# Kernel tuning notes

Hardware: AMD Instinct MI355X
Metric: run time of the kernel (lower is better)

## Reference

```python
import jax, jax.numpy as jnp
import numpy as np

N = 8192
D = 128
NUM_CLASSES = 100
EPS = 1e-8  # torch CosineSimilarity default eps


def _l2_normalize(x):
    # torch cosine sim divides by max(||x||, eps)
    n = jnp.sqrt(jnp.sum(x * x, axis=-1, keepdims=True))
    return x / jnp.maximum(n, EPS)


def _remove_diag(M):
    # [n, n] -> [n, n-1], dropping the diagonal, no boolean gather needed
    n = M.shape[0]
    return M.reshape(-1)[1:].reshape(n - 1, n + 1)[:, :-1].reshape(n, n - 1)


def setup_inputs() -> dict:
    key = jax.random.key(0)
    k1, k2, k3, k4 = jax.random.split(key, 4)
    inst_embed = jax.random.normal(k1, (N, D), dtype=jnp.float32)
    proxy = jax.random.normal(k2, (N, D), dtype=jnp.float32)
    negative_mask = jax.random.randint(k3, (NUM_CLASSES, N), 0, 2).astype(jnp.float32)
    labels = jax.random.randint(k4, (N,), 0, NUM_CLASSES, dtype=jnp.int64) if jax.config.jax_enable_x64 else jax.random.randint(k4, (N,), 0, NUM_CLASSES, dtype=jnp.int32)
    return {
        "inst_embed": inst_embed,
        "proxy": proxy,
        "negative_mask": negative_mask,
        "labels": labels,
        "temperature": jnp.float32(0.07),
        "margin": jnp.float32(0.0),
    }


def reference(inst_embed, proxy, negative_mask, labels, temperature, margin):
    xn = _l2_normalize(inst_embed)                       # [N, D]
    # pairwise cosine similarity via normalize + matmul (not NxNxD broadcast)
    sim = xn @ xn.T                                      # [N, N]
    instance_zone = jnp.exp((_remove_diag(sim) - margin) / temperature)  # [N, N-1]

    pn = _l2_normalize(proxy)
    inst2proxy_positive = jnp.exp((jnp.sum(xn * pn, axis=-1) - margin) / temperature)  # [N]

    # pos_collected_numerator == True branch
    mask = _remove_diag(negative_mask[labels])           # [N, N-1]
    numerator = jnp.sum(instance_zone * mask, axis=1) + inst2proxy_positive
    denominator = inst2proxy_positive + jnp.sum(instance_zone, axis=1)
    return -jnp.mean(jnp.log(numerator / denominator))
```

## Files before the change

kernel.cpp:

```cpp
#include <hip/hip_runtime.h>
#include <stdint.h>

#define NROWS 8192
#define DD 128
#define EPS 1e-8f
#define LOG2E 1.4426950408889634f

#define SPLIT 16
#define RPB 128
#define CPT 32
#define LDS_COL 272
#define NT ((NROWS / SPLIT) / CPT)
#define NORM_BLOCKS (NROWS / 4)
#define PACK_BLOCKS 3200

typedef __bf16 bf16x8 __attribute__((ext_vector_type(8)));
typedef float f32x4 __attribute__((ext_vector_type(4)));

__device__ __forceinline__ unsigned int f2bf(float f) {
  union { float f; unsigned int u; } v; v.f = f;
  unsigned int u = v.u;
  return (u + 0x7fffu + ((u >> 16) & 1u)) >> 16;
}
__device__ __forceinline__ float bf2f(unsigned int b) {
  union { unsigned int u; float f; } v; v.u = b << 16;
  return v.f;
}

__global__ __launch_bounds__(256) void norm_kernel(
    const float* __restrict__ x, const float* __restrict__ pr,
    const float* __restrict__ nm, const int* __restrict__ lb,
    const float* __restrict__ tptr,
    unsigned short* __restrict__ xnA, unsigned short* __restrict__ xnB,
    float* __restrict__ p, float* __restrict__ eself, float* __restrict__ mii,
    float* __restrict__ tot, float* __restrict__ msk,
    unsigned int* __restrict__ packed, float* __restrict__ out)
{
  int wave = threadIdx.x >> 6, lane = threadIdx.x & 63;
  int bx = blockIdx.x;

  if (bx >= NORM_BLOCKS) {
    int widx = (bx - NORM_BLOCKS) * 4 + wave;
    int cls = widx >> 7;
    int w64 = widx & 127;
    float v = nm[(size_t)cls * NROWS + w64 * 64 + lane];
    unsigned long long b = __ballot(v != 0.0f);
    if (lane == 0) {
      packed[cls * 256 + w64 * 2] = (unsigned int)b;
      packed[cls * 256 + w64 * 2 + 1] = (unsigned int)(b >> 32);
    }
    return;
  }

  int row = bx * 4 + wave;
  float2 xv = ((const float2*)(x + (size_t)row * DD))[lane];
  float2 pv = ((const float2*)(pr + (size_t)row * DD))[lane];
  float sx = xv.x * xv.x + xv.y * xv.y;
  float sp = pv.x * pv.x + pv.y * pv.y;
  float dp = xv.x * pv.x + xv.y * pv.y;
  #pragma unroll
  for (int m = 1; m < 64; m <<= 1) {
    sx += __shfl_xor(sx, m);
    sp += __shfl_xor(sp, m);
    dp += __shfl_xor(dp, m);
  }
  float inx = 1.f / fmaxf(sqrtf(sx), EPS);
  float inp = 1.f / fmaxf(sqrtf(sp), EPS);
  float s1 = LOG2E / tptr[0];

  unsigned int a0 = f2bf(xv.x * inx * s1), a1 = f2bf(xv.y * inx * s1);
  unsigned int b0 = f2bf(xv.x * inx),      b1 = f2bf(xv.y * inx);
  ((unsigned int*)(xnA + (size_t)row * DD))[lane] = a0 | (a1 << 16);
  ((unsigned int*)(xnB + (size_t)row * DD))[lane] = b0 | (b1 << 16);

  float ss = bf2f(a0) * bf2f(b0) + bf2f(a1) * bf2f(b1);
  #pragma unroll
  for (int m = 1; m < 64; m <<= 1) ss += __shfl_xor(ss, m);

  if (lane == 0) {
    p[row] = __builtin_amdgcn_exp2f(dp * inx * inp * s1);
    eself[row] = __builtin_amdgcn_exp2f(ss);
    mii[row] = nm[(size_t)lb[row] * NROWS + row];
    tot[row] = 0.f;
    msk[row] = 0.f;
    if (row == 0) out[0] = 0.f;
  }
}

__global__ __launch_bounds__(256, 4) void main_kernel(
    const unsigned short* __restrict__ xnA_u, const unsigned short* __restrict__ xnB_u,
    const unsigned int* __restrict__ packed, const int* __restrict__ labels,
    float* __restrict__ tot, float* __restrict__ msk)
{
  __shared__ unsigned char lds[2][CPT * LDS_COL];
  int tid = threadIdx.x;
  int wave = tid >> 6, lane = tid & 63;
  int q = lane >> 4, c = lane & 15;
  int rb0 = blockIdx.x * RPB + wave * 16;
  int rb1 = rb0 + 64;

  const bf16x8* xnvA = (const bf16x8*)xnA_u;

  bf16x8 a0[4], a1[4];
  {
    const bf16x8* b = xnvA + (size_t)(rb0 + c) * (DD / 8) + q;
    a0[0] = b[0]; a0[1] = b[4]; a0[2] = b[8]; a0[3] = b[12];
  }
  {
    const bf16x8* b = xnvA + (size_t)(rb1 + c) * (DD / 8) + q;
    a1[0] = b[0]; a1[1] = b[4]; a1[2] = b[8]; a1[3] = b[12];
  }

  int jb = blockIdx.y * (NROWS / SPLIT);

  int r0[4], r1[4];
  unsigned int offP0[4], offP1[4];
  #pragma unroll
  for (int k = 0; k < 4; k++) {
    r0[k] = rb0 + q * 4 + k;
    r1[k] = rb1 + q * 4 + k;
    offP0[k] = (unsigned int)labels[r0[k]] * 256u + (unsigned int)(jb >> 5);
    offP1[k] = (unsigned int)labels[r1[k]] * 256u + (unsigned int)(jb >> 5);
  }
  float t0[4] = {0, 0, 0, 0}, m0[4] = {0, 0, 0, 0};
  float t1[4] = {0, 0, 0, 0}, m1[4] = {0, 0, 0, 0};

  int scol = tid >> 4, schunk = tid & 15;
  const char* gB = (const char*)xnB_u;
  const char* gbase = gB + (size_t)(jb + scol) * 256 + schunk * 16;
  unsigned int ldsoff = (unsigned int)(scol * LDS_COL + schunk * 16);

  uint4 g0 = *(const uint4*)(gbase);
  uint4 g1 = *(const uint4*)(gbase + 16 * 256);
  unsigned int wn0[4], wn1[4];
  #pragma unroll
  for (int k = 0; k < 4; k++) {
    wn0[k] = packed[offP0[k]];
    wn1[k] = packed[offP1[k]];
  }
  *(uint4*)(lds[0] + ldsoff)                = g0;
  *(uint4*)(lds[0] + ldsoff + 16 * LDS_COL) = g1;
  __syncthreads();

  for (int t = 0; t < NT; t++) {
    unsigned int wc0[4], wc1[4];
    #pragma unroll
    for (int k = 0; k < 4; k++) { wc0[k] = wn0[k]; wc1[k] = wn1[k]; }

    if (t + 1 < NT) {
      const char* gb = gbase + (size_t)(t + 1) * (CPT * 256);
      g0 = *(const uint4*)(gb);
      g1 = *(const uint4*)(gb + 16 * 256);
      #pragma unroll
      for (int k = 0; k < 4; k++) {
        wn0[k] = packed[offP0[k] + t + 1];
        wn1[k] = packed[offP1[k] + t + 1];
      }
    }

    const unsigned char* buf = lds[t & 1];
    #pragma unroll
    for (int s = 0; s < 2; s++) {
      const bf16x8* bl = (const bf16x8*)(buf + (unsigned)(s * 16 + c) * LDS_COL + q * 16);
      bf16x8 b0 = bl[0], b1 = bl[4], b2 = bl[8], b3 = bl[12];

      f32x4 acc0 = {0, 0, 0, 0};
      f32x4 acc1 = {0, 0, 0, 0};
      acc0 = __builtin_amdgcn_mfma_f32_16x16x32_bf16(a0[0], b0, acc0, 0, 0, 0);
      acc1 = __builtin_amdgcn_mfma_f32_16x16x32_bf16(a1[0], b0, acc1, 0, 0, 0);
      acc0 = __builtin_amdgcn_mfma_f32_16x16x32_bf16(a0[1], b1, acc0, 0, 0, 0);
      acc1 = __builtin_amdgcn_mfma_f32_16x16x32_bf16(a1[1], b1, acc1, 0, 0, 0);
      acc0 = __builtin_amdgcn_mfma_f32_16x16x32_bf16(a0[2], b2, acc0, 0, 0, 0);
      acc1 = __builtin_amdgcn_mfma_f32_16x16x32_bf16(a1[2], b2, acc1, 0, 0, 0);
      acc0 = __builtin_amdgcn_mfma_f32_16x16x32_bf16(a0[3], b3, acc0, 0, 0, 0);
      acc1 = __builtin_amdgcn_mfma_f32_16x16x32_bf16(a1[3], b3, acc1, 0, 0, 0);

      int pos = s * 16 + c;
      #pragma unroll
      for (int k = 0; k < 4; k++) {
        float e = __builtin_amdgcn_exp2f(acc0[k]);
        t0[k] += e;
        m0[k] = fmaf(e, (float)((wc0[k] >> pos) & 1u), m0[k]);
      }
      #pragma unroll
      for (int k = 0; k < 4; k++) {
        float e = __builtin_amdgcn_exp2f(acc1[k]);
        t1[k] += e;
        m1[k] = fmaf(e, (float)((wc1[k] >> pos) & 1u), m1[k]);
      }
    }

    if (t + 1 < NT) {
      unsigned char* nb = (unsigned char*)lds[(t + 1) & 1];
      *(uint4*)(nb + ldsoff)                = g0;
      *(uint4*)(nb + ldsoff + 16 * LDS_COL) = g1;
    }
    __syncthreads();
  }

  #pragma unroll
  for (int sh = 1; sh < 16; sh <<= 1) {
    #pragma unroll
    for (int k = 0; k < 4; k++) {
      t0[k] += __shfl_xor(t0[k], sh);
      m0[k] += __shfl_xor(m0[k], sh);
      t1[k] += __shfl_xor(t1[k], sh);
      m1[k] += __shfl_xor(m1[k], sh);
    }
  }
  if (c == 0) {
    #pragma unroll
    for (int k = 0; k < 4; k++) {
      atomicAdd(&tot[r0[k]], t0[k]);
      atomicAdd(&msk[r0[k]], m0[k]);
      atomicAdd(&tot[r1[k]], t1[k]);
      atomicAdd(&msk[r1[k]], m1[k]);
    }
  }
}

__global__ __launch_bounds__(256) void loss_kernel(
    const float* __restrict__ p, const float* __restrict__ tot,
    const float* __restrict__ msk, const float* __restrict__ eself,
    const float* __restrict__ mii, float* __restrict__ out)
{
  __shared__ float sd[4];
  int r = blockIdx.x * 256 + threadIdx.x;
  float pi = p[r];
  float es = eself[r];
  float t = tot[r] - es;
  float m = msk[r] - es * mii[r];
  float v = __builtin_amdgcn_logf(pi + t) - __builtin_amdgcn_logf(pi + m);
  float s = v * (1.0f / (LOG2E * (float)NROWS));
  #pragma unroll
  for (int sh = 1; sh < 64; sh <<= 1) s += __shfl_xor(s, sh);
  int wave = threadIdx.x >> 6, lane = threadIdx.x & 63;
  if (lane == 0) sd[wave] = s;
  __syncthreads();
  if (threadIdx.x == 0) atomicAdd(out, sd[0] + sd[1] + sd[2] + sd[3]);
}

extern "C" void kernel_launch(void* const* d_in, const int* in_sizes, int n_in,
                              void* d_out, int out_size, void* d_ws, size_t ws_size,
                              hipStream_t stream) {
  const float* x  = (const float*)d_in[0];
  const float* pr = (const float*)d_in[1];
  const float* nm = (const float*)d_in[2];
  const int*   lb = (const int*)d_in[3];
  const float* tp = (const float*)d_in[4];

  char* ws = (char*)d_ws;
  unsigned short* xnA = (unsigned short*)ws;
  unsigned short* xnB = xnA + (size_t)NROWS * DD;
  float* p     = (float*)(xnB + (size_t)NROWS * DD);
  float* tot   = p + NROWS;
  float* msk   = tot + NROWS;
  float* eself = msk + NROWS;
  float* miiv  = eself + NROWS;
  unsigned int* packed = (unsigned int*)(miiv + NROWS);
  float* out = (float*)d_out;

  norm_kernel<<<NORM_BLOCKS + PACK_BLOCKS, 256, 0, stream>>>(
      x, pr, nm, lb, tp, xnA, xnB, p, eself, miiv, tot, msk, packed, out);
  main_kernel<<<dim3(NROWS / RPB, SPLIT), 256, 0, stream>>>(xnA, xnB, packed,
                                                            lb, tot, msk);
  loss_kernel<<<NROWS / 256, 256, 0, stream>>>(p, tot, msk, eself, miiv, out);
}
```

Baseline: 103.2 us.

## Double rows per block to reuse LDS column tiles across four MFMA strips

Each wave now holds four 16-row A strips instead of two, so every block covers 256 rows and each column tile staged in LDS feeds twice as many MFMAs. The mask application also changes from an int-to-float convert plus FMA to a v_bfe_i32 sign mask ANDed into the exp bits. The aim is less global and LDS traffic for B per unit of work and fewer ALU ops in the exp loop. In exchange, register pressure rises, occupancy drops to 2 blocks per launch bound, and the grid has half as many blocks in x, which may hurt latency hiding.

```diff
diff --git a/kernel.cpp b/kernel.cpp
--- a/kernel.cpp
+++ b/kernel.cpp
@@ -7,7 +7,7 @@
 #define LOG2E 1.4426950408889634f
 
 #define SPLIT 16
-#define RPB 128
+#define RPB 256
 #define CPT 32
 #define LDS_COL 272
 #define NT ((NROWS / SPLIT) / CPT)
@@ -87,7 +87,7 @@
   }
 }
 
-__global__ __launch_bounds__(256, 4) void main_kernel(
+__global__ __launch_bounds__(256, 2) void main_kernel(
     const unsigned short* __restrict__ xnA_u, const unsigned short* __restrict__ xnB_u,
     const unsigned int* __restrict__ packed, const int* __restrict__ labels,
     float* __restrict__ tot, float* __restrict__ msk)
@@ -96,34 +96,33 @@
   int tid = threadIdx.x;
   int wave = tid >> 6, lane = tid & 63;
   int q = lane >> 4, c = lane & 15;
-  int rb0 = blockIdx.x * RPB + wave * 16;
-  int rb1 = rb0 + 64;
+  int rbase = blockIdx.x * RPB + wave * 16;
 
   const bf16x8* xnvA = (const bf16x8*)xnA_u;
 
-  bf16x8 a0[4], a1[4];
-  {
-    const bf16x8* b = xnvA + (size_t)(rb0 + c) * (DD / 8) + q;
-    a0[0] = b[0]; a0[1] = b[4]; a0[2] = b[8]; a0[3] = b[12];
-  }
-  {
-    const bf16x8* b = xnvA + (size_t)(rb1 + c) * (DD / 8) + q;
-    a1[0] = b[0]; a1[1] = b[4]; a1[2] = b[8]; a1[3] = b[12];
+  bf16x8 a[4][4];
+  #pragma unroll
+  for (int st = 0; st < 4; st++) {
+    const bf16x8* b = xnvA + (size_t)(rbase + st * 64 + c) * (DD / 8) + q;
+    a[st][0] = b[0]; a[st][1] = b[4]; a[st][2] = b[8]; a[st][3] = b[12];
   }
 
   int jb = blockIdx.y * (NROWS / SPLIT);
 
-  int r0[4], r1[4];
-  unsigned int offP0[4], offP1[4];
-  #pragma unroll
-  for (int k = 0; k < 4; k++) {
-    r0[k] = rb0 + q * 4 + k;
-    r1[k] = rb1 + q * 4 + k;
-    offP0[k] = (unsigned int)labels[r0[k]] * 256u + (unsigned int)(jb >> 5);
-    offP1[k] = (unsigned int)labels[r1[k]] * 256u + (unsigned int)(jb >> 5);
-  }
-  float t0[4] = {0, 0, 0, 0}, m0[4] = {0, 0, 0, 0};
-  float t1[4] = {0, 0, 0, 0}, m1[4] = {0, 0, 0, 0};
+  unsigned int offP[4][4];
+  #pragma unroll
+  for (int st = 0; st < 4; st++) {
+    #pragma unroll
+    for (int k = 0; k < 4; k++) {
+      offP[st][k] = (unsigned int)labels[rbase + st * 64 + q * 4 + k] * 256u
+                  + (unsigned int)(jb >> 5);
+    }
+  }
+  float tacc[4][4], macc[4][4];
+  #pragma unroll
+  for (int st = 0; st < 4; st++)
+    #pragma unroll
+    for (int k = 0; k < 4; k++) { tacc[st][k] = 0.f; macc[st][k] = 0.f; }
 
   int scol = tid >> 4, schunk = tid & 15;
   const char* gB = (const char*)xnB_u;
@@ -132,30 +131,30 @@
 
   uint4 g0 = *(const uint4*)(gbase);
   uint4 g1 = *(const uint4*)(gbase + 16 * 256);
-  unsigned int wn0[4], wn1[4];
-  #pragma unroll
-  for (int k = 0; k < 4; k++) {
-    wn0[k] = packed[offP0[k]];
-    wn1[k] = packed[offP1[k]];
-  }
+  unsigned int wn[4][4];
+  #pragma unroll
+  for (int st = 0; st < 4; st++)
+    #pragma unroll
+    for (int k = 0; k < 4; k++) wn[st][k] = packed[offP[st][k]];
   *(uint4*)(lds[0] + ldsoff)                = g0;
   *(uint4*)(lds[0] + ldsoff + 16 * LDS_COL) = g1;
   __syncthreads();
 
   for (int t = 0; t < NT; t++) {
-    unsigned int wc0[4], wc1[4];
-    #pragma unroll
-    for (int k = 0; k < 4; k++) { wc0[k] = wn0[k]; wc1[k] = wn1[k]; }
+    unsigned int wc[4][4];
+    #pragma unroll
+    for (int st = 0; st < 4; st++)
+      #pragma unroll
+      for (int k = 0; k < 4; k++) wc[st][k] = wn[st][k];
 
     if (t + 1 < NT) {
       const char* gb = gbase + (size_t)(t + 1) * (CPT * 256);
       g0 = *(const uint4*)(gb);
       g1 = *(const uint4*)(gb + 16 * 256);
       #pragma unroll
-      for (int k = 0; k < 4; k++) {
-        wn0[k] = packed[offP0[k] + t + 1];
-        wn1[k] = packed[offP1[k] + t + 1];
-      }
+      for (int st = 0; st < 4; st++)
+        #pragma unroll
+        for (int k = 0; k < 4; k++) wn[st][k] = packed[offP[st][k] + t + 1];
     }
 
     const unsigned char* buf = lds[t & 1];
@@ -164,29 +163,35 @@
       const bf16x8* bl = (const bf16x8*)(buf + (unsigned)(s * 16 + c) * LDS_COL + q * 16);
       bf16x8 b0 = bl[0], b1 = bl[4], b2 = bl[8], b3 = bl[12];
 
-      f32x4 acc0 = {0, 0, 0, 0};
-      f32x4 acc1 = {0, 0, 0, 0};
-      acc0 = __builtin_amdgcn_mfma_f32_16x16x32_bf16(a0[0], b0, acc0, 0, 0, 0);
-      acc1 = __builtin_amdgcn_mfma_f32_16x16x32_bf16(a1[0], b0, acc1, 0, 0, 0);
-      acc0 = __builtin_amdgcn_mfma_f32_16x16x32_bf16(a0[1], b1, acc0, 0, 0, 0);
-      acc1 = __builtin_amdgcn_mfma_f32_16x16x32_bf16(a1[1], b1, acc1, 0, 0, 0);
-      acc0 = __builtin_amdgcn_mfma_f32_16x16x32_bf16(a0[2], b2, acc0, 0, 0, 0);
-      acc1 = __builtin_amdgcn_mfma_f32_16x16x32_bf16(a1[2], b2, acc1, 0, 0, 0);
-      acc0 = __builtin_amdgcn_mfma_f32_16x16x32_bf16(a0[3], b3, acc0, 0, 0, 0);
-      acc1 = __builtin_amdgcn_mfma_f32_16x16x32_bf16(a1[3], b3, acc1, 0, 0, 0);
+      f32x4 acc[4];
+      #pragma unroll
+      for (int st = 0; st < 4; st++) acc[st] = (f32x4){0, 0, 0, 0};
+      #pragma unroll
+      for (int st = 0; st < 4; st++)
+        acc[st] = __builtin_amdgcn_mfma_f32_16x16x32_bf16(a[st][0], b0, acc[st], 0, 0, 0);
+      #pragma unroll
+      for (int st = 0; st < 4; st++)
+        acc[st] = __builtin_amdgcn_mfma_f32_16x16x32_bf16(a[st][1], b1, acc[st], 0, 0, 0);
+      #pragma unroll
+      for (int st = 0; st < 4; st++)
+        acc[st] = __builtin_amdgcn_mfma_f32_16x16x32_bf16(a[st][2], b2, acc[st], 0, 0, 0);
+      #pragma unroll
+      for (int st = 0; st < 4; st++)
+        acc[st] = __builtin_amdgcn_mfma_f32_16x16x32_bf16(a[st][3], b3, acc[st], 0, 0, 0);
 
       int pos = s * 16 + c;
       #pragma unroll
-      for (int k = 0; k < 4; k++) {
-        float e = __builtin_amdgcn_exp2f(acc0[k]);
-        t0[k] += e;
-        m0[k] = fmaf(e, (float)((wc0[k] >> pos) & 1u), m0[k]);
-      }
-      #pragma unroll
-      for (int k = 0; k < 4; k++) {
-        float e = __builtin_amdgcn_exp2f(acc1[k]);
-        t1[k] += e;
-        m1[k] = fmaf(e, (float)((wc1[k] >> pos) & 1u), m1[k]);
+      for (int st = 0; st < 4; st++) {
+        #pragma unroll
+        for (int k = 0; k < 4; k++) {
+          float e = __builtin_amdgcn_exp2f(acc[st][k]);
+          tacc[st][k] += e;
+          int sm;
+          asm("v_bfe_i32 %0, %1, %2, 1" : "=v"(sm) : "v"(wc[st][k]), "v"(pos));
+          union { float f; int i; } u;
+          u.f = e; u.i &= sm;
+          macc[st][k] += u.f;
+        }
       }
     }
 
@@ -201,20 +206,23 @@
   #pragma unroll
   for (int sh = 1; sh < 16; sh <<= 1) {
     #pragma unroll
-    for (int k = 0; k < 4; k++) {
-      t0[k] += __shfl_xor(t0[k], sh);
-      m0[k] += __shfl_xor(m0[k], sh);
-      t1[k] += __shfl_xor(t1[k], sh);
-      m1[k] += __shfl_xor(m1[k], sh);
+    for (int st = 0; st < 4; st++) {
+      #pragma unroll
+      for (int k = 0; k < 4; k++) {
+        tacc[st][k] += __shfl_xor(tacc[st][k], sh);
+        macc[st][k] += __shfl_xor(macc[st][k], sh);
+      }
     }
   }
   if (c == 0) {
     #pragma unroll
-    for (int k = 0; k < 4; k++) {
-      atomicAdd(&tot[r0[k]], t0[k]);
-      atomicAdd(&msk[r0[k]], m0[k]);
-      atomicAdd(&tot[r1[k]], t1[k]);
-      atomicAdd(&msk[r1[k]], m1[k]);
+    for (int st = 0; st < 4; st++) {
+      #pragma unroll
+      for (int k = 0; k < 4; k++) {
+        int r = rbase + st * 64 + q * 4 + k;
+        atomicAdd(&tot[r], tacc[st][k]);
+        atomicAdd(&msk[r], macc[st][k]);
+      }
     }
   }
 }
```

Result: slower. 106.5 us (+3.2%).

## Exploit symmetry of cosine similarity matrix with triangular block schedule

Applied to the files above, without the earlier changes.

The main kernel now computes only the lower-triangular blocks of the symmetric similarity matrix, launched over a 1D triangular grid of 32x33 blocks. Each exp value feeds both the row sums and, through LDS column accumulators, the column sums, so roughly half the MFMA and exp work is dropped. Mask bits for the column direction come from extra packed-mask loads indexed by column labels. The per-element mask multiply is also replaced by a bit-extract-and-AND sequence. In exchange it adds LDS atomics, extra global atomics and uneven per-block work on the diagonal.

```diff
diff --git a/kernel.cpp b/kernel.cpp
--- a/kernel.cpp
+++ b/kernel.cpp
@@ -6,11 +6,12 @@
 #define EPS 1e-8f
 #define LOG2E 1.4426950408889634f
 
-#define SPLIT 16
-#define RPB 128
+#define SPLITQ 32
+#define CPW 256
 #define CPT 32
+#define NT (CPW / CPT)
+#define NBLK (SPLITQ * (SPLITQ + 1))
 #define LDS_COL 272
-#define NT ((NROWS / SPLIT) / CPT)
 #define NORM_BLOCKS (NROWS / 4)
 #define PACK_BLOCKS 3200
 
@@ -93,10 +94,24 @@
     float* __restrict__ tot, float* __restrict__ msk)
 {
   __shared__ unsigned char lds[2][CPT * LDS_COL];
+  __shared__ float colacc[2][CPW];
   int tid = threadIdx.x;
   int wave = tid >> 6, lane = tid & 63;
   int q = lane >> 4, c = lane & 15;
-  int rb0 = blockIdx.x * RPB + wave * 16;
+
+  int n = blockIdx.x;
+  int by = (int)((sqrtf((float)(4 * n + 1)) - 1.0f) * 0.5f);
+  while (by * (by + 1) > n) by--;
+  while ((by + 1) * (by + 2) <= n) by++;
+  int bx = n - by * (by + 1);
+
+  int rblock = bx * 128;
+  int jb = by * CPW;
+  int diag = (by == (bx >> 1));
+  int tstart = diag ? 4 * (bx & 1) : 0;
+  int tcol0  = diag ? tstart + 4 : 0;
+
+  int rb0 = rblock + wave * 16;
   int rb1 = rb0 + 64;
 
   const bf16x8* xnvA = (const bf16x8*)xnA_u;
@@ -111,14 +126,16 @@
     a1[0] = b[0]; a1[1] = b[4]; a1[2] = b[8]; a1[3] = b[12];
   }
 
-  int jb = blockIdx.y * (NROWS / SPLIT);
-
+  ((float*)colacc)[tid] = 0.f;
+  ((float*)colacc)[tid + 256] = 0.f;
+
+  int q4 = q * 4;
   int r0[4], r1[4];
   unsigned int offP0[4], offP1[4];
   #pragma unroll
   for (int k = 0; k < 4; k++) {
-    r0[k] = rb0 + q * 4 + k;
-    r1[k] = rb1 + q * 4 + k;
+    r0[k] = rb0 + q4 + k;
+    r1[k] = rb1 + q4 + k;
     offP0[k] = (unsigned int)labels[r0[k]] * 256u + (unsigned int)(jb >> 5);
     offP1[k] = (unsigned int)labels[r1[k]] * 256u + (unsigned int)(jb >> 5);
   }
@@ -130,22 +147,38 @@
   const char* gbase = gB + (size_t)(jb + scol) * 256 + schunk * 16;
   unsigned int ldsoff = (unsigned int)(scol * LDS_COL + schunk * 16);
 
-  uint4 g0 = *(const uint4*)(gbase);
-  uint4 g1 = *(const uint4*)(gbase + 16 * 256);
+  unsigned int rw = (unsigned int)(rblock >> 5);
+  unsigned int wsel = (unsigned int)(wave >> 1);
+  int base01 = (wave & 1) * 16 + q4;
+
+  uint4 g0 = *(const uint4*)(gbase + (size_t)tstart * (CPT * 256));
+  uint4 g1 = *(const uint4*)(gbase + (size_t)tstart * (CPT * 256) + 16 * 256);
   unsigned int wn0[4], wn1[4];
   #pragma unroll
   for (int k = 0; k < 4; k++) {
-    wn0[k] = packed[offP0[k]];
-    wn1[k] = packed[offP1[k]];
-  }
-  *(uint4*)(lds[0] + ldsoff)                = g0;
-  *(uint4*)(lds[0] + ldsoff + 16 * LDS_COL) = g1;
+    wn0[k] = packed[offP0[k] + tstart];
+    wn1[k] = packed[offP1[k] + tstart];
+  }
+  unsigned int ncw[4] = {0, 0, 0, 0};
+  if (tstart >= tcol0) {
+    unsigned int lab0 = (unsigned int)labels[jb + tstart * 32 + c];
+    unsigned int lab1 = (unsigned int)labels[jb + tstart * 32 + 16 + c];
+    ncw[0] = packed[lab0 * 256u + rw + wsel];
+    ncw[1] = packed[lab0 * 256u + rw + 2u + wsel];
+    ncw[2] = packed[lab1 * 256u + rw + wsel];
+    ncw[3] = packed[lab1 * 256u + rw + 2u + wsel];
+  }
+  *(uint4*)(lds[tstart & 1] + ldsoff)                = g0;
+  *(uint4*)(lds[tstart & 1] + ldsoff + 16 * LDS_COL) = g1;
   __syncthreads();
 
-  for (int t = 0; t < NT; t++) {
-    unsigned int wc0[4], wc1[4];
+  for (int t = tstart; t < NT; t++) {
+    unsigned int wc0[4], wc1[4], ccw[4];
     #pragma unroll
     for (int k = 0; k < 4; k++) { wc0[k] = wn0[k]; wc1[k] = wn1[k]; }
+    #pragma unroll
+    for (int k = 0; k < 4; k++) ccw[k] = ncw[k];
+    int docol = (t >= tcol0);
 
     if (t + 1 < NT) {
       const char* gb = gbase + (size_t)(t + 1) * (CPT * 256);
@@ -155,6 +188,14 @@
       for (int k = 0; k < 4; k++) {
         wn0[k] = packed[offP0[k] + t + 1];
         wn1[k] = packed[offP1[k] + t + 1];
+      }
+      if (t + 1 >= tcol0) {
+        unsigned int lab0 = (unsigned int)labels[jb + (t + 1) * 32 + c];
+        unsigned int lab1 = (unsigned int)labels[jb + (t + 1) * 32 + 16 + c];
+        ncw[0] = packed[lab0 * 256u + rw + wsel];
+        ncw[1] = packed[lab0 * 256u + rw + 2u + wsel];
+        ncw[2] = packed[lab1 * 256u + rw + wsel];
+        ncw[3] = packed[lab1 * 256u + rw + 2u + wsel];
       }
     }
 
@@ -176,17 +217,50 @@
       acc1 = __builtin_amdgcn_mfma_f32_16x16x32_bf16(a1[3], b3, acc1, 0, 0, 0);
 
       int pos = s * 16 + c;
+      unsigned int cwS0 = s ? ccw[2] : ccw[0];
+      unsigned int cwS1 = s ? ccw[3] : ccw[1];
+      float colT = 0.f, colM = 0.f;
       #pragma unroll
       for (int k = 0; k < 4; k++) {
         float e = __builtin_amdgcn_exp2f(acc0[k]);
         t0[k] += e;
-        m0[k] = fmaf(e, (float)((wc0[k] >> pos) & 1u), m0[k]);
+        int smr;
+        asm("v_bfe_i32 %0, %1, %2, 1" : "=v"(smr) : "v"(wc0[k]), "v"(pos));
+        union { float f; int i; } ur; ur.f = e; ur.i &= smr;
+        m0[k] += ur.f;
+        if (docol) {
+          colT += e;
+          int pc = base01 + k;
+          int smc;
+          asm("v_bfe_i32 %0, %1, %2, 1" : "=v"(smc) : "v"(cwS0), "v"(pc));
+          union { float f; int i; } uc; uc.f = e; uc.i &= smc;
+          colM += uc.f;
+        }
       }
       #pragma unroll
       for (int k = 0; k < 4; k++) {
         float e = __builtin_amdgcn_exp2f(acc1[k]);
         t1[k] += e;
-        m1[k] = fmaf(e, (float)((wc1[k] >> pos) & 1u), m1[k]);
+        int smr;
+        asm("v_bfe_i32 %0, %1, %2, 1" : "=v"(smr) : "v"(wc1[k]), "v"(pos));
+        union { float f; int i; } ur; ur.f = e; ur.i &= smr;
+        m1[k] += ur.f;
+        if (docol) {
+          colT += e;
+          int pc = base01 + k;
+          int smc;
+          asm("v_bfe_i32 %0, %1, %2, 1" : "=v"(smc) : "v"(cwS1), "v"(pc));
+          union { float f; int i; } uc; uc.f = e; uc.i &= smc;
+          colM += uc.f;
+        }
+      }
+      if (docol) {
+        colT += __shfl_xor(colT, 16); colT += __shfl_xor(colT, 32);
+        colM += __shfl_xor(colM, 16); colM += __shfl_xor(colM, 32);
+        if (q == 0) {
+          atomicAdd(&colacc[0][t * 32 + pos], colT);
+          atomicAdd(&colacc[1][t * 32 + pos], colM);
+        }
       }
     }
 
@@ -216,6 +290,12 @@
       atomicAdd(&tot[r1[k]], t1[k]);
       atomicAdd(&msk[r1[k]], m1[k]);
     }
+  }
+
+  int ci = tid;
+  if (ci >= tcol0 * 32) {
+    atomicAdd(&tot[jb + ci], colacc[0][ci]);
+    atomicAdd(&msk[jb + ci], colacc[1][ci]);
   }
 }
 
@@ -262,7 +342,6 @@
 
   norm_kernel<<<NORM_BLOCKS + PACK_BLOCKS, 256, 0, stream>>>(
       x, pr, nm, lb, tp, xnA, xnB, p, eself, miiv, tot, msk, packed, out);
-  main_kernel<<<dim3(NROWS / RPB, SPLIT), 256, 0, stream>>>(xnA, xnB, packed,
-                                                            lb, tot, msk);
+  main_kernel<<<NBLK, 256, 0, stream>>>(xnA, xnB, packed, lb, tot, msk);
   loss_kernel<<<NROWS / 256, 256, 0, stream>>>(p, tot, msk, eself, miiv, out);
 }
```

Measured after the change: 145.0 us. +40.4%, slower.

## Use direct global-to-LDS loads with triple buffering and XOR swizzle

Applied to the files above, without the earlier changes.

Replaces the register-staged double-buffered B-tile loads with global_load_lds direct transfers into a three-deep LDS ring, prefetching two tiles ahead and waiting with explicit vmcnt counters before each barrier. The padded LDS layout is replaced by an XOR swizzle on 16-byte chunks to avoid bank conflicts without padding. The mask accumulation now uses a v_bfe_i32 sign mask and a bitwise AND instead of an int-to-float conversion and FMA. The aim is to remove VGPR staging and LDS store instructions and to deepen the overlap of loads with MFMA work, at the cost of more LDS and fragile manual waitcnt handling. The last iterations issue redundant wrapped loads so the vmcnt bookkeeping stays uniform.

```diff
diff --git a/kernel.cpp b/kernel.cpp
--- a/kernel.cpp
+++ b/kernel.cpp
@@ -9,7 +9,7 @@
 #define SPLIT 16
 #define RPB 128
 #define CPT 32
-#define LDS_COL 272
+#define TILEB (CPT * 256)
 #define NT ((NROWS / SPLIT) / CPT)
 #define NORM_BLOCKS (NROWS / 4)
 #define PACK_BLOCKS 3200
@@ -25,6 +25,12 @@
 __device__ __forceinline__ float bf2f(unsigned int b) {
   union { unsigned int u; float f; } v; v.u = b << 16;
   return v.f;
+}
+
+__device__ __forceinline__ void gl16(const void* g, void* l) {
+  __builtin_amdgcn_global_load_lds(
+      (const __attribute__((address_space(1))) unsigned int*)g,
+      (__attribute__((address_space(3))) unsigned int*)l, 16, 0, 0);
 }
 
 __global__ __launch_bounds__(256) void norm_kernel(
@@ -92,7 +98,7 @@
     const unsigned int* __restrict__ packed, const int* __restrict__ labels,
     float* __restrict__ tot, float* __restrict__ msk)
 {
-  __shared__ unsigned char lds[2][CPT * LDS_COL];
+  __shared__ unsigned char lds[3][TILEB];
   int tid = threadIdx.x;
   int wave = tid >> 6, lane = tid & 63;
   int q = lane >> 4, c = lane & 15;
@@ -113,12 +119,13 @@
 
   int jb = blockIdx.y * (NROWS / SPLIT);
 
+  int q4 = q * 4;
   int r0[4], r1[4];
   unsigned int offP0[4], offP1[4];
   #pragma unroll
   for (int k = 0; k < 4; k++) {
-    r0[k] = rb0 + q * 4 + k;
-    r1[k] = rb1 + q * 4 + k;
+    r0[k] = rb0 + q4 + k;
+    r1[k] = rb1 + q4 + k;
     offP0[k] = (unsigned int)labels[r0[k]] * 256u + (unsigned int)(jb >> 5);
     offP1[k] = (unsigned int)labels[r1[k]] * 256u + (unsigned int)(jb >> 5);
   }
@@ -126,43 +133,61 @@
   float t1[4] = {0, 0, 0, 0}, m1[4] = {0, 0, 0, 0};
 
   int scol = tid >> 4, schunk = tid & 15;
+  int sx7 = scol & 7;
   const char* gB = (const char*)xnB_u;
-  const char* gbase = gB + (size_t)(jb + scol) * 256 + schunk * 16;
-  unsigned int ldsoff = (unsigned int)(scol * LDS_COL + schunk * 16);
-
-  uint4 g0 = *(const uint4*)(gbase);
-  uint4 g1 = *(const uint4*)(gbase + 16 * 256);
+  const char* gsrc = gB + (size_t)(jb + scol) * 256 + (schunk ^ sx7) * 16;
+  unsigned dof0 = (unsigned)(wave * 1024);
+  unsigned dof1 = dof0 + 4096;
+
   unsigned int wn0[4], wn1[4];
   #pragma unroll
   for (int k = 0; k < 4; k++) {
     wn0[k] = packed[offP0[k]];
     wn1[k] = packed[offP1[k]];
   }
-  *(uint4*)(lds[0] + ldsoff)                = g0;
-  *(uint4*)(lds[0] + ldsoff + 16 * LDS_COL) = g1;
-  __syncthreads();
+
+  gl16(gsrc,                     lds[0] + dof0);
+  gl16(gsrc + 16 * 256,          lds[0] + dof1);
+  gl16(gsrc + TILEB,             lds[1] + dof0);
+  gl16(gsrc + TILEB + 16 * 256,  lds[1] + dof1);
+  __builtin_amdgcn_sched_barrier(0);
+  asm volatile("s_waitcnt vmcnt(2)" ::: "memory");
+  __builtin_amdgcn_sched_barrier(0);
+  __builtin_amdgcn_s_barrier();
+
+  unsigned cur = 0, nxt = 1, nx2 = 2;
 
   for (int t = 0; t < NT; t++) {
     unsigned int wc0[4], wc1[4];
     #pragma unroll
     for (int k = 0; k < 4; k++) { wc0[k] = wn0[k]; wc1[k] = wn1[k]; }
 
-    if (t + 1 < NT) {
-      const char* gb = gbase + (size_t)(t + 1) * (CPT * 256);
-      g0 = *(const uint4*)(gb);
-      g1 = *(const uint4*)(gb + 16 * 256);
-      #pragma unroll
-      for (int k = 0; k < 4; k++) {
-        wn0[k] = packed[offP0[k] + t + 1];
-        wn1[k] = packed[offP1[k] + t + 1];
-      }
-    }
-
-    const unsigned char* buf = lds[t & 1];
+    int tn = (t + 1 < NT) ? (t + 1) : (NT - 1);
+    #pragma unroll
+    for (int k = 0; k < 4; k++) {
+      wn0[k] = packed[offP0[k] + tn];
+      wn1[k] = packed[offP1[k] + tn];
+    }
+
+    {
+      int t2 = t + 2; if (t2 >= NT) t2 -= NT;
+      const char* gs2 = gsrc + (size_t)t2 * TILEB;
+      unsigned char* db = &lds[0][0] + nx2 * TILEB;
+      gl16(gs2,            db + dof0);
+      gl16(gs2 + 16 * 256, db + dof1);
+    }
+    __builtin_amdgcn_sched_barrier(0);
+
+    const unsigned char* buf = &lds[0][0] + cur * TILEB;
     #pragma unroll
     for (int s = 0; s < 2; s++) {
-      const bf16x8* bl = (const bf16x8*)(buf + (unsigned)(s * 16 + c) * LDS_COL + q * 16);
-      bf16x8 b0 = bl[0], b1 = bl[4], b2 = bl[8], b3 = bl[12];
+      unsigned colb = (unsigned)((s * 16 + c) * 256);
+      unsigned x7 = (unsigned)(c & 7);
+      const unsigned char* bp = buf + colb;
+      bf16x8 b0 = *(const bf16x8*)(bp + ((((unsigned)q)      ^ x7) << 4));
+      bf16x8 b1 = *(const bf16x8*)(bp + ((((unsigned)q + 4)  ^ x7) << 4));
+      bf16x8 b2 = *(const bf16x8*)(bp + ((((unsigned)q + 8)  ^ x7) << 4));
+      bf16x8 b3 = *(const bf16x8*)(bp + ((((unsigned)q + 12) ^ x7) << 4));
 
       f32x4 acc0 = {0, 0, 0, 0};
       f32x4 acc1 = {0, 0, 0, 0};
@@ -180,22 +205,29 @@
       for (int k = 0; k < 4; k++) {
         float e = __builtin_amdgcn_exp2f(acc0[k]);
         t0[k] += e;
-        m0[k] = fmaf(e, (float)((wc0[k] >> pos) & 1u), m0[k]);
+        int sm;
+        asm("v_bfe_i32 %0, %1, %2, 1" : "=v"(sm) : "v"(wc0[k]), "v"(pos));
+        union { float f; int i; } u;
+        u.f = e; u.i &= sm;
+        m0[k] += u.f;
       }
       #pragma unroll
       for (int k = 0; k < 4; k++) {
         float e = __builtin_amdgcn_exp2f(acc1[k]);
         t1[k] += e;
-        m1[k] = fmaf(e, (float)((wc1[k] >> pos) & 1u), m1[k]);
+        int sm;
+        asm("v_bfe_i32 %0, %1, %2, 1" : "=v"(sm) : "v"(wc1[k]), "v"(pos));
+        union { float f; int i; } u;
+        u.f = e; u.i &= sm;
+        m1[k] += u.f;
       }
     }
 
-    if (t + 1 < NT) {
-      unsigned char* nb = (unsigned char*)lds[(t + 1) & 1];
-      *(uint4*)(nb + ldsoff)                = g0;
-      *(uint4*)(nb + ldsoff + 16 * LDS_COL) = g1;
-    }
-    __syncthreads();
+    asm volatile("s_waitcnt vmcnt(2)" ::: "memory");
+    __builtin_amdgcn_sched_barrier(0);
+    __builtin_amdgcn_s_barrier();
+
+    unsigned tmp = cur; cur = nxt; nxt = nx2; nx2 = tmp;
   }
 
   #pragma unroll
```

Measured after the change: 109.1 us. 1.06x slower.
